# Kernel optimization log

Measured on AMD Instinct MI355X. Metric: run time of the kernel, lower is better.

## Reference

```python
import jax, jax.numpy as jnp
import numpy as np

D_MODEL = 1024
N_HEAD = 16


def setup_inputs() -> dict:
    key = jax.random.key(0)
    ks = jax.random.split(key, 12)
    B, S, D = 4, 2048, D_MODEL
    scale = 1.0 / np.sqrt(D)
    inp = {
        "Q": jax.random.normal(ks[0], (B, S, D), jnp.float32),
        "K": jax.random.normal(ks[1], (B, S, D), jnp.float32),
        "V": jax.random.normal(ks[2], (B, S, D), jnp.float32),
        "Wq": jax.random.normal(ks[3], (D, D), jnp.float32) * scale,
        "bq": jax.random.normal(ks[4], (D,), jnp.float32) * scale,
        "Wk": jax.random.normal(ks[5], (D, D), jnp.float32) * scale,
        "bk": jax.random.normal(ks[6], (D,), jnp.float32) * scale,
        "Wv": jax.random.normal(ks[7], (D, D), jnp.float32) * scale,
        "bv": jax.random.normal(ks[8], (D,), jnp.float32) * scale,
        "Wo": jax.random.normal(ks[9], (D, D), jnp.float32) * scale,
        "bo": jax.random.normal(ks[10], (D,), jnp.float32) * scale,
    }
    return inp


def _split_heads(x, n_head):
    B, S, D = x.shape
    return x.reshape(B, S, n_head, D // n_head).transpose(0, 2, 1, 3)  # [B,H,S,dh]


def reference(Q, K, V, Wq, bq, Wk, bk, Wv, bv, Wo, bo):
    # torch Linear: x @ W.T + b
    q = _split_heads(Q @ Wq.T + bq, N_HEAD)
    k = _split_heads(K @ Wk.T + bk, N_HEAD)
    v = _split_heads(V @ Wv.T + bv, N_HEAD)
    d_k = k.shape[-1]
    score = jnp.einsum('bhqd,bhkd->bhqk', q, k) / jnp.sqrt(jnp.float32(d_k))
    attn = jax.nn.softmax(score, axis=-1)
    out = jnp.einsum('bhqk,bhkd->bhqd', attn, v)  # [B,H,S,dh]
    B, H, S, dh = out.shape
    out = out.transpose(0, 2, 1, 3).reshape(B, S, H * dh)
    return out @ Wo.T + bo
```

## Files before the change

kernel.cpp:

```cpp
#include <hip/hip_runtime.h>
#include <math.h>

#define D_MODEL 1024
#define N_HEAD  16
#define DH      64
#define SEQ     2048
#define BATCH   4
#define BH      (BATCH*N_HEAD)
#define MROWS   (BATCH*SEQ)

typedef __attribute__((ext_vector_type(8)))  short          s16x8;
typedef __attribute__((ext_vector_type(8)))  unsigned short u16x8;
typedef __attribute__((ext_vector_type(4)))  unsigned short u16x4;
typedef __attribute__((ext_vector_type(4)))  float          f32x4;
typedef __attribute__((ext_vector_type(16))) float          f32x16;
typedef __attribute__((ext_vector_type(4)))  unsigned int   u32x4;

#define QSCALE 0.18033688f

typedef const __attribute__((address_space(1))) unsigned int gu32;
typedef __attribute__((address_space(3))) unsigned int lu32;
#define GLOAD_LDS16(g, l) __builtin_amdgcn_global_load_lds((gu32*)(g), (lu32*)(l), 16, 0, 0)

__device__ __forceinline__ unsigned short f2bf(float x) {
    unsigned int u = __float_as_uint(x);
    u += 0x7FFFu + ((u >> 16) & 1u);
    return (unsigned short)(u >> 16);
}

__device__ __forceinline__ unsigned int cvtpk_bf16(float lo, float hi) {
    unsigned int r;
    asm("v_cvt_pk_bf16_f32 %0, %1, %2" : "=v"(r) : "v"(lo), "v"(hi));
    return r;
}

__device__ __forceinline__ float exp2_asm(float x) {
    float r;
    asm("v_exp_f32 %0, %1" : "=v"(r) : "v"(x));
    return r;
}

__device__ __forceinline__ float max3f(float a, float b, float c) {
    float r;
    asm("v_max3_f32 %0, %1, %2, %3" : "=v"(r) : "v"(a), "v"(b), "v"(c));
    return r;
}

__global__ __launch_bounds__(256) void conv_w4(const float* __restrict__ w0,
                                               const float* __restrict__ w1,
                                               const float* __restrict__ w2,
                                               const float* __restrict__ w3,
                                               unsigned short* __restrict__ o0,
                                               unsigned short* __restrict__ o1,
                                               unsigned short* __restrict__ o2,
                                               unsigned short* __restrict__ o3)
{
    const float* w; unsigned short* o;
    switch (blockIdx.y) {
        case 0:  w = w0; o = o0; break;
        case 1:  w = w1; o = o1; break;
        case 2:  w = w2; o = o2; break;
        default: w = w3; o = o3; break;
    }
    int i = blockIdx.x * 256 + threadIdx.x;
    const float4* p = (const float4*)w + (size_t)i * 2;
    float4 a = p[0], b = p[1];
    u16x8 v;
    v[0] = f2bf(a.x); v[1] = f2bf(a.y); v[2] = f2bf(a.z); v[3] = f2bf(a.w);
    v[4] = f2bf(b.x); v[5] = f2bf(b.y); v[6] = f2bf(b.z); v[7] = f2bf(b.w);
    *((u16x8*)o + i) = v;
}

template<int MODE, bool AF32>
__global__ __launch_bounds__(256) void gemm_bt(const void* __restrict__ Av,
                                               const unsigned short* __restrict__ W,
                                               const float* __restrict__ bias,
                                               unsigned short* __restrict__ outb,
                                               float* __restrict__ outf,
                                               float oscale)
{
    __shared__ short As[128 * 64];
    __shared__ short Bs[128 * 64];
    const int tid = threadIdx.x;
    const int w = tid >> 6, l = tid & 63;
    const int lr = l & 15, lg = l >> 4;
    const int wm = w >> 1, wn = w & 1;
    const int r0 = blockIdx.x * 128, c0 = blockIdx.y * 128;
    const int srow = tid >> 3;
    const int sc8  = tid & 7;

    f32x4 zz = {0.f, 0.f, 0.f, 0.f};
    f32x4 acc[4][4];
    #pragma unroll
    for (int i = 0; i < 4; ++i)
        #pragma unroll
        for (int j = 0; j < 4; ++j) acc[i][j] = zz;

    const unsigned short* Ab = (const unsigned short*)Av;
    const float*          Af = (const float*)Av;

    const int lrow8 = l >> 3;
    const int lslot = l & 7;
    size_t bsrc[4];
    #pragma unroll
    for (int p = 0; p < 4; ++p)
        bsrc[p] = ((size_t)(c0 + w * 32 + p * 8 + lrow8) * 1024 + (size_t)((lslot ^ lrow8) * 8)) * 2;

    u16x8 ar[4];
    float4 arf[4][2];
    #pragma unroll
    for (int p = 0; p < 4; ++p) {
        int row = p * 32 + srow;
        if (AF32) {
            arf[p][0] = *(const float4*)(Af + (size_t)(r0 + row) * 1024 + sc8 * 8);
            arf[p][1] = *(const float4*)(Af + (size_t)(r0 + row) * 1024 + sc8 * 8 + 4);
        } else {
            ar[p] = *(const u16x8*)(Ab + (size_t)(r0 + row) * 1024 + sc8 * 8);
        }
    }

    for (int ks = 0; ks < 16; ++ks) {
        __syncthreads();
        #pragma unroll
        for (int p = 0; p < 4; ++p)
            GLOAD_LDS16((const char*)W + bsrc[p] + (size_t)ks * 128, &Bs[(w * 32 + p * 8) * 64]);
        #pragma unroll
        for (int p = 0; p < 4; ++p) {
            int row = p * 32 + srow;
            if (AF32) {
                u32x4 wd;
                wd[0] = cvtpk_bf16(arf[p][0].x, arf[p][0].y);
                wd[1] = cvtpk_bf16(arf[p][0].z, arf[p][0].w);
                wd[2] = cvtpk_bf16(arf[p][1].x, arf[p][1].y);
                wd[3] = cvtpk_bf16(arf[p][1].z, arf[p][1].w);
                *(u16x8*)&As[row * 64 + ((sc8 ^ (row & 7)) * 8)] = __builtin_bit_cast(u16x8, wd);
            } else {
                *(u16x8*)&As[row * 64 + ((sc8 ^ (row & 7)) * 8)] = ar[p];
            }
        }
        __syncthreads();
        if (ks < 15) {
            int k0 = (ks + 1) * 64;
            #pragma unroll
            for (int p = 0; p < 4; ++p) {
                int row = p * 32 + srow;
                if (AF32) {
                    arf[p][0] = *(const float4*)(Af + (size_t)(r0 + row) * 1024 + k0 + sc8 * 8);
                    arf[p][1] = *(const float4*)(Af + (size_t)(r0 + row) * 1024 + k0 + sc8 * 8 + 4);
                } else {
                    ar[p] = *(const u16x8*)(Ab + (size_t)(r0 + row) * 1024 + k0 + sc8 * 8);
                }
            }
        }
        #pragma unroll
        for (int t = 0; t < 2; ++t) {
            const int k8 = lg + 4 * t;
            s16x8 af[4], bw[4];
            #pragma unroll
            for (int i = 0; i < 4; ++i) {
                int rowa = wm * 64 + i * 16 + lr;
                af[i] = *(const s16x8*)&As[rowa * 64 + ((k8 ^ (rowa & 7)) * 8)];
                int rowb = wn * 64 + i * 16 + lr;
                bw[i] = *(const s16x8*)&Bs[rowb * 64 + ((k8 ^ (rowb & 7)) * 8)];
            }
            #pragma unroll
            for (int i = 0; i < 4; ++i)
                #pragma unroll
                for (int j = 0; j < 4; ++j)
                    acc[i][j] = __builtin_amdgcn_mfma_f32_16x16x32_bf16(af[i], bw[j], acc[i][j], 0, 0, 0);
        }
    }

    #pragma unroll
    for (int i = 0; i < 4; ++i) {
        #pragma unroll
        for (int j = 0; j < 4; ++j) {
            const int colb = c0 + wn * 64 + j * 16 + lr;
            const float bv = bias[colb];
            if (MODE == 2) {
                const int row = r0 + wm * 64 + i * 16 + lg * 4;
                const int b = row >> 11, s = row & 2047;
                const int h = colb >> 6, d = colb & 63;
                u16x4 pv;
                pv[0] = f2bf((acc[i][j][0] + bv) * oscale);
                pv[1] = f2bf((acc[i][j][1] + bv) * oscale);
                pv[2] = f2bf((acc[i][j][2] + bv) * oscale);
                pv[3] = f2bf((acc[i][j][3] + bv) * oscale);
                *(u16x4*)(outb + ((size_t)(b * N_HEAD + h) * DH + d) * SEQ + s) = pv;
            } else {
                #pragma unroll
                for (int rg = 0; rg < 4; ++rg) {
                    const int row = r0 + wm * 64 + i * 16 + lg * 4 + rg;
                    const float v = acc[i][j][rg] + bv;
                    if (MODE == 0) {
                        outf[(size_t)row * D_MODEL + colb] = v;
                    } else {
                        const int b = row >> 11, s = row & 2047;
                        const int h = colb >> 6, d = colb & 63;
                        outb[((size_t)(b * N_HEAD + h) * SEQ + s) * DH + d] = f2bf(v * oscale);
                    }
                }
            }
        }
    }
}

__global__ __launch_bounds__(256, 4) void flash_attn_mfma32(const unsigned short* __restrict__ qb,
                                                            const unsigned short* __restrict__ kb,
                                                            const unsigned short* __restrict__ vtb,
                                                            unsigned short* __restrict__ aob)
{
    __shared__ u16x8 Kt[2][512];
    __shared__ u16x8 Vt[2][512];

    const int tid = threadIdx.x;
    const int w = tid >> 6, l = tid & 63;
    const int q32 = l & 31;
    const int h = l >> 5;

    const int wg   = blockIdx.x;
    const int xcd  = wg & 7;
    const int slot = wg >> 3;
    const int bh   = xcd * 8 + (slot >> 4);
    const int qt   = slot & 15;

    const unsigned short* qh = qb + (size_t)bh * SEQ * DH;
    const unsigned short* kh = kb + (size_t)bh * SEQ * DH;
    const unsigned short* vh = vtb + (size_t)bh * DH * SEQ;

    const int qrow = qt * 128 + w * 32 + q32;

    s16x8 qf[4];
    #pragma unroll
    for (int ks = 0; ks < 4; ++ks)
        qf[ks] = *(const s16x8*)(qh + (size_t)qrow * DH + ks * 16 + h * 8);

    f32x16 O[2];
    #pragma unroll
    for (int r = 0; r < 16; ++r) { O[0][r] = 0.f; O[1][r] = 0.f; }
    float m = 0.f, lsum = 0.f;

    const int srow = tid >> 3;
    const int sc8  = tid & 7;

    u16x8 kreg[2], vreg[2];
    #pragma unroll
    for (int p = 0; p < 2; ++p) {
        int rr = p * 32 + srow;
        kreg[p] = *(const u16x8*)(kh + (size_t)rr * DH + sc8 * 8);
        vreg[p] = *(const u16x8*)(vh + (size_t)rr * SEQ + sc8 * 8);
    }
    #pragma unroll
    for (int p = 0; p < 2; ++p) {
        int rr = p * 32 + srow;
        Kt[0][sc8 * 64 + (rr ^ sc8)] = kreg[p];
        Vt[0][sc8 * 64 + (rr ^ sc8)] = vreg[p];
    }
    __syncthreads();

    int buf = 0;
    for (int kv = 0; kv < SEQ / 64; ++kv) {
        if (kv < SEQ / 64 - 1) {
            const int s0 = (kv + 1) * 64;
            #pragma unroll
            for (int p = 0; p < 2; ++p) {
                int rr = p * 32 + srow;
                kreg[p] = *(const u16x8*)(kh + (size_t)(s0 + rr) * DH + sc8 * 8);
                vreg[p] = *(const u16x8*)(vh + (size_t)rr * SEQ + s0 + sc8 * 8);
            }
        }

        f32x16 SC[2];
        #pragma unroll
        for (int r = 0; r < 16; ++r) { SC[0][r] = -m; SC[1][r] = -m; }
        __builtin_amdgcn_s_setprio(1);
        #pragma unroll
        for (int ks = 0; ks < 4; ++ks) {
            const int chunk = 2 * ks + h;
            #pragma unroll
            for (int c = 0; c < 2; ++c) {
                const int row = c * 32 + q32;
                s16x8 kf = __builtin_bit_cast(s16x8, Kt[buf][chunk * 64 + (row ^ chunk)]);
                SC[c] = __builtin_amdgcn_mfma_f32_32x32x16_bf16(kf, qf[ks], SC[c], 0, 0, 0);
            }
        }
        __builtin_amdgcn_s_setprio(0);

        #define GETSC(i) ((i) < 16 ? SC[0][(i)] : SC[1][(i) - 16])
        float t0[11];
        #pragma unroll
        for (int r = 0; r < 10; ++r)
            t0[r] = max3f(GETSC(3 * r), GETSC(3 * r + 1), GETSC(3 * r + 2));
        t0[10] = fmaxf(GETSC(30), GETSC(31));
        float u0 = max3f(t0[0], t0[1], t0[2]);
        float u1 = max3f(t0[3], t0[4], t0[5]);
        float u2 = max3f(t0[6], t0[7], t0[8]);
        float u3 = fmaxf(t0[9], t0[10]);
        float rmb_l = fmaxf(max3f(u0, u1, u2), u3);
        float rmb = fmaxf(rmb_l, __shfl_xor(rmb_l, 32, 64));
        #undef GETSC

        if (!__all(rmb <= 8.0f)) {
            const float delta = fmaxf(rmb, 0.f);
            const float fold = exp2_asm(-delta);
            lsum *= fold;
            O[0] *= fold;
            O[1] *= fold;
            m += delta;
            #pragma unroll
            for (int c = 0; c < 2; ++c)
                #pragma unroll
                for (int r = 0; r < 16; ++r)
                    SC[c][r] -= delta;
        }

        #pragma unroll
        for (int c = 0; c < 2; ++c)
            #pragma unroll
            for (int r = 0; r < 16; ++r)
                SC[c][r] = exp2_asm(SC[c][r]);

        float s0a[8];
        #pragma unroll
        for (int r = 0; r < 8; ++r)
            s0a[r] = (SC[0][r] + SC[0][r + 8]) + (SC[1][r] + SC[1][r + 8]);
        #pragma unroll
        for (int d = 4; d; d >>= 1)
            #pragma unroll
            for (int r = 0; r < d; ++r) s0a[r] += s0a[r + d];
        lsum += s0a[0] + __shfl_xor(s0a[0], 32, 64);

        s16x8 pa[4];
        #pragma unroll
        for (int s = 0; s < 4; ++s) {
            const int c = s >> 1, rb = (s & 1) * 8;
            unsigned int a0 = cvtpk_bf16(SC[c][rb + 0], SC[c][rb + 1]);
            unsigned int a1 = cvtpk_bf16(SC[c][rb + 2], SC[c][rb + 3]);
            unsigned int b0 = cvtpk_bf16(SC[c][rb + 4], SC[c][rb + 5]);
            unsigned int b1 = cvtpk_bf16(SC[c][rb + 6], SC[c][rb + 7]);
            asm volatile("v_permlane32_swap_b32 %0, %1" : "+v"(a0), "+v"(b0));
            asm volatile("v_permlane32_swap_b32 %0, %1" : "+v"(a1), "+v"(b1));
            u32x4 wd;
            wd[0] = a0;
            wd[1] = a1;
            wd[2] = b0;
            wd[3] = b1;
            pa[s] = __builtin_bit_cast(s16x8, wd);
        }

        __builtin_amdgcn_s_setprio(1);
        #pragma unroll
        for (int s = 0; s < 4; ++s) {
            const int chunk = 2 * s + h;
            #pragma unroll
            for (int c = 0; c < 2; ++c) {
                const int row = c * 32 + q32;
                s16x8 vf = __builtin_bit_cast(s16x8, Vt[buf][chunk * 64 + (row ^ chunk)]);
                O[c] = __builtin_amdgcn_mfma_f32_32x32x16_bf16(vf, pa[s], O[c], 0, 0, 0);
            }
        }
        __builtin_amdgcn_s_setprio(0);

        if (kv < SEQ / 64 - 1) {
            #pragma unroll
            for (int p = 0; p < 2; ++p) {
                int rr = p * 32 + srow;
                Kt[buf ^ 1][sc8 * 64 + (rr ^ sc8)] = kreg[p];
                Vt[buf ^ 1][sc8 * 64 + (rr ^ sc8)] = vreg[p];
            }
            __syncthreads();
            buf ^= 1;
        }
    }

    const float inv = 1.0f / lsum;
    const int b = bh >> 4, head = bh & 15;
    unsigned short* obase = aob + ((size_t)b * SEQ + qrow) * D_MODEL + head * DH;
    #pragma unroll
    for (int c = 0; c < 2; ++c) {
        #pragma unroll
        for (int rq = 0; rq < 4; ++rq) {
            const int d0 = 8 * rq + 4 * h + 32 * c;
            u16x4 pv;
            #pragma unroll
            for (int j = 0; j < 4; ++j) pv[j] = f2bf(O[c][rq * 4 + j] * inv);
            *(u16x4*)(obase + d0) = pv;
        }
    }
}

extern "C" void kernel_launch(void* const* d_in, const int* in_sizes, int n_in,
                              void* d_out, int out_size, void* d_ws, size_t ws_size,
                              hipStream_t stream)
{
    const float* Q  = (const float*)d_in[0];
    const float* K  = (const float*)d_in[1];
    const float* V  = (const float*)d_in[2];
    const float* Wq = (const float*)d_in[3];
    const float* bq = (const float*)d_in[4];
    const float* Wk = (const float*)d_in[5];
    const float* bk = (const float*)d_in[6];
    const float* Wv = (const float*)d_in[7];
    const float* bv = (const float*)d_in[8];
    const float* Wo = (const float*)d_in[9];
    const float* bo = (const float*)d_in[10];

    const size_t PER = (size_t)MROWS * D_MODEL;
    const size_t WSZ = (size_t)D_MODEL * D_MODEL;
    unsigned short* wqb = (unsigned short*)d_ws;
    unsigned short* wkb = wqb + WSZ;
    unsigned short* wvb = wkb + WSZ;
    unsigned short* wob = wvb + WSZ;
    unsigned short* qb2 = wob + WSZ;
    unsigned short* kb2 = qb2 + PER;
    unsigned short* vtb = kb2 + PER;
    unsigned short* aob = vtb + PER;

    dim3 gg(MROWS / 128, D_MODEL / 128);

    conv_w4<<<dim3(512, 4), 256, 0, stream>>>(Wq, Wk, Wv, Wo, wqb, wkb, wvb, wob);

    gemm_bt<1, true><<<gg, 256, 0, stream>>>(Q, wqb, bq, qb2, nullptr, QSCALE);
    gemm_bt<1, true><<<gg, 256, 0, stream>>>(K, wkb, bk, kb2, nullptr, 1.0f);
    gemm_bt<2, true><<<gg, 256, 0, stream>>>(V, wvb, bv, vtb, nullptr, 1.0f);

    flash_attn_mfma32<<<dim3(16 * BH), 256, 0, stream>>>(qb2, kb2, vtb, aob);

    gemm_bt<0, false><<<gg, 256, 0, stream>>>(aob, wob, bo, nullptr, (float*)d_out, 1.0f);
}
```

Before: 221.7 us.

## Double-buffer LDS tiles in projection GEMM to overlap loads with MFMA

Splits the A and B shared-memory tiles into two buffers. The next K-slice is staged (async global-to-LDS for W, register prefetch for A) into the alternate buffer while MFMAs run on the current one. This cuts the two barriers per iteration to one and hides load latency behind compute. In exchange LDS use doubles to 64KB per block, which may reduce occupancy.

```diff
diff --git a/kernel.cpp b/kernel.cpp
--- a/kernel.cpp
+++ b/kernel.cpp
@@ -79,8 +79,8 @@
                                                float* __restrict__ outf,
                                                float oscale)
 {
-    __shared__ short As[128 * 64];
-    __shared__ short Bs[128 * 64];
+    __shared__ short As[2][128 * 64];
+    __shared__ short Bs[2][128 * 64];
     const int tid = threadIdx.x;
     const int w = tid >> 6, l = tid & 63;
     const int lr = l & 15, lg = l >> 4;
@@ -108,6 +108,7 @@
 
     u16x8 ar[4];
     float4 arf[4][2];
+
     #pragma unroll
     for (int p = 0; p < 4; ++p) {
         int row = p * 32 + srow;
@@ -118,37 +119,67 @@
             ar[p] = *(const u16x8*)(Ab + (size_t)(r0 + row) * 1024 + sc8 * 8);
         }
     }
-
+    #pragma unroll
+    for (int p = 0; p < 4; ++p)
+        GLOAD_LDS16((const char*)W + bsrc[p], &Bs[0][(w * 32 + p * 8) * 64]);
+    #pragma unroll
+    for (int p = 0; p < 4; ++p) {
+        int row = p * 32 + srow;
+        if (AF32) {
+            u32x4 wd;
+            wd[0] = cvtpk_bf16(arf[p][0].x, arf[p][0].y);
+            wd[1] = cvtpk_bf16(arf[p][0].z, arf[p][0].w);
+            wd[2] = cvtpk_bf16(arf[p][1].x, arf[p][1].y);
+            wd[3] = cvtpk_bf16(arf[p][1].z, arf[p][1].w);
+            *(u16x8*)&As[0][row * 64 + ((sc8 ^ (row & 7)) * 8)] = __builtin_bit_cast(u16x8, wd);
+        } else {
+            *(u16x8*)&As[0][row * 64 + ((sc8 ^ (row & 7)) * 8)] = ar[p];
+        }
+    }
+    #pragma unroll
+    for (int p = 0; p < 4; ++p) {
+        int row = p * 32 + srow;
+        if (AF32) {
+            arf[p][0] = *(const float4*)(Af + (size_t)(r0 + row) * 1024 + 64 + sc8 * 8);
+            arf[p][1] = *(const float4*)(Af + (size_t)(r0 + row) * 1024 + 64 + sc8 * 8 + 4);
+        } else {
+            ar[p] = *(const u16x8*)(Ab + (size_t)(r0 + row) * 1024 + 64 + sc8 * 8);
+        }
+    }
+    __syncthreads();
+
+    int buf = 0;
     for (int ks = 0; ks < 16; ++ks) {
-        __syncthreads();
-        #pragma unroll
-        for (int p = 0; p < 4; ++p)
-            GLOAD_LDS16((const char*)W + bsrc[p] + (size_t)ks * 128, &Bs[(w * 32 + p * 8) * 64]);
-        #pragma unroll
-        for (int p = 0; p < 4; ++p) {
-            int row = p * 32 + srow;
-            if (AF32) {
-                u32x4 wd;
-                wd[0] = cvtpk_bf16(arf[p][0].x, arf[p][0].y);
-                wd[1] = cvtpk_bf16(arf[p][0].z, arf[p][0].w);
-                wd[2] = cvtpk_bf16(arf[p][1].x, arf[p][1].y);
-                wd[3] = cvtpk_bf16(arf[p][1].z, arf[p][1].w);
-                *(u16x8*)&As[row * 64 + ((sc8 ^ (row & 7)) * 8)] = __builtin_bit_cast(u16x8, wd);
-            } else {
-                *(u16x8*)&As[row * 64 + ((sc8 ^ (row & 7)) * 8)] = ar[p];
-            }
-        }
-        __syncthreads();
         if (ks < 15) {
-            int k0 = (ks + 1) * 64;
+            #pragma unroll
+            for (int p = 0; p < 4; ++p)
+                GLOAD_LDS16((const char*)W + bsrc[p] + (size_t)(ks + 1) * 128,
+                            &Bs[buf ^ 1][(w * 32 + p * 8) * 64]);
             #pragma unroll
             for (int p = 0; p < 4; ++p) {
                 int row = p * 32 + srow;
                 if (AF32) {
-                    arf[p][0] = *(const float4*)(Af + (size_t)(r0 + row) * 1024 + k0 + sc8 * 8);
-                    arf[p][1] = *(const float4*)(Af + (size_t)(r0 + row) * 1024 + k0 + sc8 * 8 + 4);
+                    u32x4 wd;
+                    wd[0] = cvtpk_bf16(arf[p][0].x, arf[p][0].y);
+                    wd[1] = cvtpk_bf16(arf[p][0].z, arf[p][0].w);
+                    wd[2] = cvtpk_bf16(arf[p][1].x, arf[p][1].y);
+                    wd[3] = cvtpk_bf16(arf[p][1].z, arf[p][1].w);
+                    *(u16x8*)&As[buf ^ 1][row * 64 + ((sc8 ^ (row & 7)) * 8)] = __builtin_bit_cast(u16x8, wd);
                 } else {
-                    ar[p] = *(const u16x8*)(Ab + (size_t)(r0 + row) * 1024 + k0 + sc8 * 8);
+                    *(u16x8*)&As[buf ^ 1][row * 64 + ((sc8 ^ (row & 7)) * 8)] = ar[p];
+                }
+            }
+            if (ks < 14) {
+                int k0 = (ks + 2) * 64;
+                #pragma unroll
+                for (int p = 0; p < 4; ++p) {
+                    int row = p * 32 + srow;
+                    if (AF32) {
+                        arf[p][0] = *(const float4*)(Af + (size_t)(r0 + row) * 1024 + k0 + sc8 * 8);
+                        arf[p][1] = *(const float4*)(Af + (size_t)(r0 + row) * 1024 + k0 + sc8 * 8 + 4);
+                    } else {
+                        ar[p] = *(const u16x8*)(Ab + (size_t)(r0 + row) * 1024 + k0 + sc8 * 8);
+                    }
                 }
             }
         }
@@ -159,15 +190,19 @@
             #pragma unroll
             for (int i = 0; i < 4; ++i) {
                 int rowa = wm * 64 + i * 16 + lr;
-                af[i] = *(const s16x8*)&As[rowa * 64 + ((k8 ^ (rowa & 7)) * 8)];
+                af[i] = *(const s16x8*)&As[buf][rowa * 64 + ((k8 ^ (rowa & 7)) * 8)];
                 int rowb = wn * 64 + i * 16 + lr;
-                bw[i] = *(const s16x8*)&Bs[rowb * 64 + ((k8 ^ (rowb & 7)) * 8)];
+                bw[i] = *(const s16x8*)&Bs[buf][rowb * 64 + ((k8 ^ (rowb & 7)) * 8)];
             }
             #pragma unroll
             for (int i = 0; i < 4; ++i)
                 #pragma unroll
                 for (int j = 0; j < 4; ++j)
                     acc[i][j] = __builtin_amdgcn_mfma_f32_16x16x32_bf16(af[i], bw[j], acc[i][j], 0, 0, 0);
+        }
+        if (ks < 15) {
+            __syncthreads();
+            buf ^= 1;
         }
     }
 
```

Measured after the change: 217.0 us. -2.1%, faster.
